# Kernel tuning notes

Hardware: AMD Instinct MI355X
Metric: run time of the kernel (lower is better)

## Reference

```python
import jax, jax.numpy as jnp
import numpy as np

HQ, HK, D = 16, 4, 64
WINDOW = 1024  # sliding-window left size; right=0 (causal)
GATE_CH = 12
RMS_EPS = 1e-8


def rms_norm(x):
    return x * jax.lax.rsqrt(jnp.mean(x * x, axis=-1, keepdims=True) + RMS_EPS)


def apply_rope(x, cos, sin):
    # x: [B,T,H,D]; cos/sin: [T,D//2] broadcast to [1,T,1,D//2]
    x1, x2 = jnp.split(x, 2, axis=-1)
    c = cos[None, :, None, :]
    s = sin[None, :, None, :]
    return jnp.concatenate([x1 * c - x2 * s, x1 * s + x2 * c], axis=-1)


def setup_inputs() -> dict:
    key = jax.random.key(0)
    ks = jax.random.split(key, 7)
    B, T, E = 2, 2048, HQ * D
    x = jax.random.normal(ks[0], (B, T, E), jnp.float32)
    value_embeds = jax.random.normal(ks[1], (B, T, HK * D), jnp.float32)
    # rope cache: angles for half the head dim
    inv_freq = 1.0 / (10000.0 ** (jnp.arange(D // 2, dtype=jnp.float32) / (D // 2)))
    ang = jnp.arange(T, dtype=jnp.float32)[:, None] * inv_freq[None, :]
    rope_cos = jnp.cos(ang)
    rope_sin = jnp.sin(ang)
    std = (3.0 ** 0.5) * (E ** -0.5)
    w_qkv = jax.random.uniform(ks[2], ((HQ + 2 * HK) * D, E), jnp.float32, -std, std)
    w_gate = jax.random.normal(ks[3], (HK, GATE_CH), jnp.float32) * 0.02
    w_o = jax.random.normal(ks[4], (E, E), jnp.float32) * 0.02
    return {"x": x, "value_embeds": value_embeds, "rope_cos": rope_cos,
            "rope_sin": rope_sin, "w_qkv": w_qkv, "w_gate": w_gate, "w_o": w_o}


def reference(x, value_embeds, rope_cos, rope_sin, w_qkv, w_gate, w_o):
    B, T, E = x.shape
    groups = HQ // HK
    qkv = jnp.einsum('bte,fe->btf', x, w_qkv).reshape(B, T, HQ + 2 * HK, D)
    q = qkv[:, :, :HQ, :]
    k = qkv[:, :, HQ:HQ + HK, :]
    v = qkv[:, :, HQ + HK:, :]
    # value-embedding gating
    ve = value_embeds.reshape(B, T, HK, D)
    gate = 3.0 * jax.nn.sigmoid(jnp.einsum('btc,hc->bth', x[..., :GATE_CH], w_gate))
    v = v + gate[..., None] * ve
    # rope + qk-norm
    q = rms_norm(apply_rope(q, rope_cos, rope_sin))
    k = rms_norm(apply_rope(k, rope_cos, rope_sin))
    # GQA: repeat kv heads
    k_rep = jnp.repeat(k, groups, axis=2)  # [B,T,HQ,D]
    v_rep = jnp.repeat(v, groups, axis=2)
    scale = 1.0 / jnp.sqrt(jnp.float32(D))
    scores = jnp.einsum('bqhd,bkhd->bhqk', q, k_rep) * scale
    i = jnp.arange(T)[:, None]
    j = jnp.arange(T)[None, :]
    mask = (j <= i) & (j >= i - WINDOW)  # causal + sliding window
    scores = jnp.where(mask[None, None], scores, jnp.float32(-1e30))
    attn = jax.nn.softmax(scores, axis=-1)
    out = jnp.einsum('bhqk,bkhd->bqhd', attn, v_rep).reshape(B, T, E)
    out = jnp.einsum('bte,fe->btf', out, w_o)
    return out
```

## Files before the change

### kernel.cpp

```cpp
#include <hip/hip_runtime.h>
#include <math.h>

#define T_LEN 2048
#define NB 2
#define E_DIM 1024
#define F_DIM 1536
#define HQn 16
#define HKn 4
#define Dh 64
#define WIN 1024
#define GATE_CH 12
#define PS 72
#define PSV 68
#define CS 73

typedef unsigned short u16;
typedef unsigned int u32;
typedef __attribute__((ext_vector_type(8))) short bf16x8;
typedef __attribute__((ext_vector_type(4))) short bf16x4;
typedef __attribute__((ext_vector_type(4))) float f32x4;

#if __has_builtin(__builtin_amdgcn_mfma_f32_16x16x16bf16_1k)
#define MFMA16(A, B, C) __builtin_amdgcn_mfma_f32_16x16x16bf16_1k(A, B, C, 0, 0, 0)
#elif __has_builtin(__builtin_amdgcn_mfma_f32_16x16x16_bf16)
#define MFMA16(A, B, C) __builtin_amdgcn_mfma_f32_16x16x16_bf16(A, B, C, 0, 0, 0)
#else
static __device__ __forceinline__ f32x4 mfma16_asm(bf16x4 a, bf16x4 b, f32x4 c) {
  f32x4 d;
  asm volatile("s_nop 1\n\tv_mfma_f32_16x16x16_bf16 %0, %1, %2, %3\n\ts_nop 7\n\ts_nop 7"
               : "=v"(d) : "v"(a), "v"(b), "v"(c));
  return d;
}
#define MFMA16(A, B, C) mfma16_asm(A, B, C)
#endif

__device__ __forceinline__ u16 f2bf(float f) {
  union { float f; unsigned int u; } v; v.f = f;
  unsigned int u = v.u + 0x7FFF + ((v.u >> 16) & 1);
  return (u16)(u >> 16);
}
__device__ __forceinline__ float bf2f(u16 h) {
  union { unsigned int u; float f; } v; v.u = ((unsigned int)h) << 16;
  return v.f;
}
__device__ __forceinline__ u32 pack_bf2(float hi, float lo) {
  union { float f; u32 u; } a, b; a.f = hi; b.f = lo;
  return __builtin_amdgcn_perm(a.u + 0x8000u, b.u + 0x8000u, 0x07060302u);
}
__device__ __forceinline__ void async_copy16(const void* g, void* l) {
  __builtin_amdgcn_global_load_lds(
      (const __attribute__((address_space(1))) unsigned int*)g,
      (__attribute__((address_space(3))) unsigned int*)l, 16, 0, 0);
}

__global__ __launch_bounds__(256) void cvt_all(
    const float4* __restrict__ x, const float4* __restrict__ wqkv,
    const float4* __restrict__ wo, uint2* __restrict__ xb,
    uint2* __restrict__ wqb, uint2* __restrict__ wob)
{
  int blk = blockIdx.x;
  const float4* in; uint2* out; int i;
  if (blk < 4096)       { in = x;    out = xb;  i = blk * 256 + threadIdx.x; }
  else if (blk < 5632)  { in = wqkv; out = wqb; i = (blk - 4096) * 256 + threadIdx.x; }
  else                  { in = wo;   out = wob; i = (blk - 5632) * 256 + threadIdx.x; }
  float4 v = in[i];
  uint2 o;
  o.x = (unsigned)f2bf(v.x) | ((unsigned)f2bf(v.y) << 16);
  o.y = (unsigned)f2bf(v.z) | ((unsigned)f2bf(v.w) << 16);
  out[i] = o;
}

__global__ __launch_bounds__(256) void gemm_qkv(
    const u16* __restrict__ A, const u16* __restrict__ B,
    const float* __restrict__ x, const float* __restrict__ ve,
    const float* __restrict__ rcos, const float* __restrict__ rsin,
    const float* __restrict__ wg,
    u16* __restrict__ qa, u16* __restrict__ ka, u16* __restrict__ vt)
{
  constexpr int K = E_DIM;
  __shared__ u16 smem[24576];
  __shared__ float gateL[128];
  u16* As = smem;
  u16* Bs = smem + 16384;
  u16* Ct = smem;
  const int tid = threadIdx.x;
  const int wave = tid >> 6, lane = tid & 63;
  const int quad = lane >> 4, lanelow = lane & 15;
  const int row0 = blockIdx.x * 128;
  const int h    = blockIdx.y;
  const int col0 = h * 64;
  const int wm = (wave >> 1) * 64, wn = (wave & 1) * 32;

  f32x4 acc[4][2];
#pragma unroll
  for (int i = 0; i < 4; ++i)
#pragma unroll
    for (int j = 0; j < 2; ++j) acc[i][j] = (f32x4){0.f, 0.f, 0.f, 0.f};

  auto stage = [&](int buf, int k0) {
#pragma unroll
    for (int s = 0; s < 4; ++s) {
      int slot = s * 256 + tid;
      int r = slot >> 3, g = (slot & 7) ^ (r & 7);
      async_copy16(A + (size_t)(row0 + r) * K + k0 + g * 8,
                   &As[buf * 8192 + slot * 8]);
    }
#pragma unroll
    for (int s = 0; s < 2; ++s) {
      int slot = s * 256 + tid;
      int r = slot >> 3, g = (slot & 7) ^ (r & 7);
      async_copy16(B + (size_t)(col0 + r) * K + k0 + g * 8,
                   &Bs[buf * 4096 + slot * 8]);
    }
  };

  stage(0, 0);
  __syncthreads();
  int cur = 0;
  for (int k0 = 0; k0 < K; k0 += 64) {
    if (k0 + 64 < K) stage(cur ^ 1, k0 + 64);
#pragma unroll
    for (int kk = 0; kk < 2; ++kk) {
      bf16x8 a[4], b[2];
#pragma unroll
      for (int i = 0; i < 4; ++i) {
        int r = wm + i * 16 + lanelow;
        a[i] = *(const bf16x8*)&As[cur * 8192 + r * 64 + (((kk * 4 + quad) ^ (r & 7)) * 8)];
      }
#pragma unroll
      for (int j = 0; j < 2; ++j) {
        int r = wn + j * 16 + lanelow;
        b[j] = *(const bf16x8*)&Bs[cur * 4096 + r * 64 + (((kk * 4 + quad) ^ (r & 7)) * 8)];
      }
#pragma unroll
      for (int i = 0; i < 4; ++i)
#pragma unroll
        for (int j = 0; j < 2; ++j)
          acc[i][j] = __builtin_amdgcn_mfma_f32_16x16x32_bf16(a[i], b[j], acc[i][j], 0, 0, 0);
    }
    __syncthreads();
    cur ^= 1;
  }

#pragma unroll
  for (int i = 0; i < 4; ++i)
#pragma unroll
    for (int j = 0; j < 2; ++j)
#pragma unroll
      for (int reg = 0; reg < 4; ++reg) {
        int row = wm + i * 16 + quad * 4 + reg;
        int col = wn + j * 16 + lanelow;
        Ct[row * CS + col] = f2bf(acc[i][j][reg]);
      }
  __syncthreads();

  if (h < HQn + HKn) {
    const bool isq = (h < HQn);
    const int half = lane & 31;
    for (int t = wave * 32; t < wave * 32 + 32; ++t) {
      int tok = row0 + t;
      int tt = tok & (T_LEN - 1);
      float c = rcos[tt * 32 + half], s = rsin[tt * 32 + half];
      float x1 = bf2f(Ct[t * CS + half]);
      float x2 = bf2f(Ct[t * CS + half + 32]);
      float y = (lane < 32) ? (x1 * c - x2 * s) : (x1 * s + x2 * c);
      float ss = y * y;
#pragma unroll
      for (int o = 32; o; o >>= 1) ss += __shfl_xor(ss, o, 64);
      float v = y * rsqrtf(ss * (1.f / Dh) + 1e-8f);
      if (isq)
        qa[((size_t)tok * HQn + h) * Dh + lane] = f2bf(v * 0.1803368801f);
      else
        ka[((size_t)tok * HKn + (h - HQn)) * Dh + lane] = f2bf(v);
    }
  } else {
    const int hk = h - (HQn + HKn);
    if (tid < 128) {
      int tok = row0 + tid;
      float g = 0.f;
#pragma unroll
      for (int c = 0; c < GATE_CH; ++c)
        g += x[(size_t)tok * E_DIM + c] * wg[hk * GATE_CH + c];
      gateL[tid] = 3.f / (1.f + __expf(-g));
    }
    __syncthreads();
    for (int t = wave * 32; t < wave * 32 + 32; ++t) {
      int tok = row0 + t;
      float val = bf2f(Ct[t * CS + lane]) +
                  gateL[t] * ve[(size_t)tok * (HKn * Dh) + hk * Dh + lane];
      Ct[t * CS + lane] = f2bf(val);
    }
    __syncthreads();
    int d = tid >> 2, tseg = (tid & 3) * 32;
    int tokbase = row0 + tseg;
    int b = tokbase >> 11;
    int tloc = tokbase & (T_LEN - 1);
    u16 tmp[32];
#pragma unroll
    for (int e = 0; e < 32; ++e) tmp[e] = Ct[(tseg + e) * CS + d];
    u16* dst = vt + ((size_t)(b * HKn + hk) * Dh + d) * T_LEN + tloc;
#pragma unroll
    for (int p = 0; p < 4; ++p)
      *(uint4*)(dst + p * 8) = *(uint4*)&tmp[p * 8];
  }
}

template<int BM, int BN, int STORE_BF16>
__global__ __launch_bounds__(256) void gemm_async(
    const u16* __restrict__ A, const u16* __restrict__ B,
    void* __restrict__ Cv, int M, int N, int K)
{
  constexpr int MI = BM / 32, NJ = BN / 32;
  constexpr int NSA = BM / 32;
  constexpr int NSB = BN / 32;
  __shared__ u16 As[2][BM * 64];
  __shared__ u16 Bs[2][BN * 64];
  const int tid = threadIdx.x;
  const int wave = tid >> 6, lane = tid & 63;
  const int quad = lane >> 4, lanelow = lane & 15;
  const int row0 = blockIdx.x * BM;
  const int col0 = blockIdx.y * BN;
  const int wm = (wave >> 1) * (BM / 2), wn = (wave & 1) * (BN / 2);

  f32x4 acc[MI][NJ];
#pragma unroll
  for (int i = 0; i < MI; ++i)
#pragma unroll
    for (int j = 0; j < NJ; ++j) acc[i][j] = (f32x4){0.f, 0.f, 0.f, 0.f};

  auto stage = [&](int buf, int k0) {
#pragma unroll
    for (int s = 0; s < NSA; ++s) {
      int slot = s * 256 + tid;
      int r = slot >> 3, g = (slot & 7) ^ (r & 7);
      async_copy16(A + (size_t)(row0 + r) * K + k0 + g * 8, &As[buf][slot * 8]);
    }
#pragma unroll
    for (int s = 0; s < NSB; ++s) {
      int slot = s * 256 + tid;
      int r = slot >> 3, g = (slot & 7) ^ (r & 7);
      async_copy16(B + (size_t)(col0 + r) * K + k0 + g * 8, &Bs[buf][slot * 8]);
    }
  };

  stage(0, 0);
  __syncthreads();
  int cur = 0;
  for (int k0 = 0; k0 < K; k0 += 64) {
    if (k0 + 64 < K) stage(cur ^ 1, k0 + 64);
#pragma unroll
    for (int kk = 0; kk < 2; ++kk) {
      bf16x8 a[MI], b[NJ];
#pragma unroll
      for (int i = 0; i < MI; ++i) {
        int r = wm + i * 16 + lanelow;
        a[i] = *(const bf16x8*)&As[cur][r * 64 + (((kk * 4 + quad) ^ (r & 7)) * 8)];
      }
#pragma unroll
      for (int j = 0; j < NJ; ++j) {
        int r = wn + j * 16 + lanelow;
        b[j] = *(const bf16x8*)&Bs[cur][r * 64 + (((kk * 4 + quad) ^ (r & 7)) * 8)];
      }
#pragma unroll
      for (int i = 0; i < MI; ++i)
#pragma unroll
        for (int j = 0; j < NJ; ++j)
          acc[i][j] = __builtin_amdgcn_mfma_f32_16x16x32_bf16(a[i], b[j], acc[i][j], 0, 0, 0);
    }
    __syncthreads();
    cur ^= 1;
  }

#pragma unroll
  for (int i = 0; i < MI; ++i)
#pragma unroll
    for (int j = 0; j < NJ; ++j) {
      int r = row0 + wm + i * 16 + quad * 4;
      int c = col0 + wn + j * 16 + lanelow;
#pragma unroll
      for (int reg = 0; reg < 4; ++reg) {
        if (STORE_BF16)
          ((u16*)Cv)[(size_t)(r + reg) * N + c] = f2bf(acc[i][j][reg]);
        else
          ((float*)Cv)[(size_t)(r + reg) * N + c] = acc[i][j][reg];
      }
    }
}

__global__ __launch_bounds__(256) void attn_mfma(
    const u16* __restrict__ qa, const u16* __restrict__ ka,
    const u16* __restrict__ vt_g, u16* __restrict__ att)
{
  __shared__ u16 Ks[2][64 * PS];
  __shared__ u16 Vt[2][64 * PSV];
  const int bx = blockIdx.x, h = blockIdx.y, b = blockIdx.z;
  const int j5 = bx & 7;
  const int t5 = (bx >> 3) & 3;
  const int tu = (t5 + (h >> 3) + 2 * b) & 3;
  const int qt = (tu == 0) ? j5
               : (tu == 1) ? (15 - j5)
                           : (16 + 2 * j5 + (tu & 1));
  const int hk = h >> 2;
  const int qb = qt * 64;
  const int tid = threadIdx.x;
  const int wave = tid >> 6, lane = tid & 63;
  const int quad = lane >> 4, lanelow = lane & 15;

  bf16x8 aQ[2];
#pragma unroll
  for (int kk = 0; kk < 2; ++kk)
    aQ[kk] = *(const bf16x8*)(qa +
        ((size_t)(b * T_LEN + qb + wave * 16 + lanelow) * HQn + h) * Dh +
        kk * 32 + quad * 8);

  f32x4 O[4];
  float l = 0.f;
#pragma unroll
  for (int dt = 0; dt < 4; ++dt) O[dt] = (f32x4){0.f, 0.f, 0.f, 0.f};

  const int kt0 = (qt >= 16) ? qt - 16 : 0;
  const int kt1 = qt;

  const int sr0 = tid >> 3,         sc0 = (tid & 7) * 8;
  const int sr1 = (tid + 256) >> 3, sc1 = ((tid + 256) & 7) * 8;
  const u16* kg = ka + (size_t)(b * T_LEN) * (HKn * Dh) + hk * Dh;
  const u16* vg = vt_g + (size_t)(b * HKn + hk) * Dh * T_LEN;

  {
    const int kb = kt0 * 64;
    uint4 k0 = *(const uint4*)(kg + (size_t)(kb + sr0) * (HKn * Dh) + sc0);
    uint4 k1 = *(const uint4*)(kg + (size_t)(kb + sr1) * (HKn * Dh) + sc1);
    uint4 v0 = *(const uint4*)(vg + (size_t)sr0 * T_LEN + kb + sc0);
    uint4 v1 = *(const uint4*)(vg + (size_t)sr1 * T_LEN + kb + sc1);
    *(uint4*)&Ks[0][sr0 * PS + sc0] = k0;
    *(uint4*)&Ks[0][sr1 * PS + sc1] = k1;
    *(uint2*)&Vt[0][sr0 * PSV + sc0]     = make_uint2(v0.x, v0.y);
    *(uint2*)&Vt[0][sr0 * PSV + sc0 + 4] = make_uint2(v0.z, v0.w);
    *(uint2*)&Vt[0][sr1 * PSV + sc1]     = make_uint2(v1.x, v1.y);
    *(uint2*)&Vt[0][sr1 * PSV + sc1 + 4] = make_uint2(v1.z, v1.w);
  }

  for (int kt = kt0; kt <= kt1; ++kt) {
    const int buf = (kt - kt0) & 1;
    const int kb = kt * 64;
    uint4 k0, k1, v0, v1;
    const bool more = (kt < kt1);
    if (more) {
      const int nb = kb + 64;
      k0 = *(const uint4*)(kg + (size_t)(nb + sr0) * (HKn * Dh) + sc0);
      k1 = *(const uint4*)(kg + (size_t)(nb + sr1) * (HKn * Dh) + sc1);
      v0 = *(const uint4*)(vg + (size_t)sr0 * T_LEN + nb + sc0);
      v1 = *(const uint4*)(vg + (size_t)sr1 * T_LEN + nb + sc1);
    }
    __syncthreads();

    f32x4 St[4];
#pragma unroll
    for (int jt = 0; jt < 4; ++jt) {
      bf16x8 aK0 = *(const bf16x8*)&Ks[buf][(jt * 16 + lanelow) * PS + quad * 8];
      bf16x8 aK1 = *(const bf16x8*)&Ks[buf][(jt * 16 + lanelow) * PS + 32 + quad * 8];
      f32x4 acc = (f32x4){-12.f, -12.f, -12.f, -12.f};
      acc = __builtin_amdgcn_mfma_f32_16x16x32_bf16(aK0, aQ[0], acc, 0, 0, 0);
      acc = __builtin_amdgcn_mfma_f32_16x16x32_bf16(aK1, aQ[1], acc, 0, 0, 0);
      St[jt] = acc;
    }
    if (kt == kt1) {
#pragma unroll
      for (int jt = 0; jt < 4; ++jt)
#pragma unroll
        for (int rr = 0; rr < 4; ++rr) {
          int ig = qb + wave * 16 + lanelow;
          int jg = kb + jt * 16 + quad * 4 + rr;
          if (jg > ig) St[jt][rr] = -1e30f;
        }
    } else if (kt == kt0 && qt >= 16) {
#pragma unroll
      for (int jt = 0; jt < 4; ++jt)
#pragma unroll
        for (int rr = 0; rr < 4; ++rr) {
          int ig = qb + wave * 16 + lanelow;
          int jg = kb + jt * 16 + quad * 4 + rr;
          if (jg < ig - WIN) St[jt][rr] = -1e30f;
        }
    }
    bf16x4 Pt[4];
#pragma unroll
    for (int jt = 0; jt < 4; ++jt) {
      float p0 = __builtin_amdgcn_exp2f(St[jt][0]);
      float p1 = __builtin_amdgcn_exp2f(St[jt][1]);
      float p2 = __builtin_amdgcn_exp2f(St[jt][2]);
      float p3 = __builtin_amdgcn_exp2f(St[jt][3]);
      l += (p0 + p1) + (p2 + p3);
      union { uint2 u; bf16x4 v; } pu;
      pu.u.x = pack_bf2(p1, p0);
      pu.u.y = pack_bf2(p3, p2);
      Pt[jt] = pu.v;
    }
#pragma unroll
    for (int dt = 0; dt < 4; ++dt)
#pragma unroll
      for (int jt = 0; jt < 4; ++jt) {
        bf16x4 aV = *(const bf16x4*)&Vt[buf][(dt * 16 + lanelow) * PSV + jt * 16 + quad * 4];
        O[dt] = MFMA16(aV, Pt[jt], O[dt]);
      }
    if (more) {
      const int nbuf = buf ^ 1;
      *(uint4*)&Ks[nbuf][sr0 * PS + sc0] = k0;
      *(uint4*)&Ks[nbuf][sr1 * PS + sc1] = k1;
      *(uint2*)&Vt[nbuf][sr0 * PSV + sc0]     = make_uint2(v0.x, v0.y);
      *(uint2*)&Vt[nbuf][sr0 * PSV + sc0 + 4] = make_uint2(v0.z, v0.w);
      *(uint2*)&Vt[nbuf][sr1 * PSV + sc1]     = make_uint2(v1.x, v1.y);
      *(uint2*)&Vt[nbuf][sr1 * PSV + sc1 + 4] = make_uint2(v1.z, v1.w);
    }
  }

  {
    float s = l;
    s += __shfl_xor(s, 16, 64);
    s += __shfl_xor(s, 32, 64);
    float inv = 1.f / s;
    int qg = qb + wave * 16 + lanelow;
    u16* obase = att + (size_t)(b * T_LEN + qg) * E_DIM + h * Dh;
#pragma unroll
    for (int dt = 0; dt < 4; ++dt) {
      bf16x4 ov;
      ov[0] = (short)f2bf(O[dt][0] * inv);
      ov[1] = (short)f2bf(O[dt][1] * inv);
      ov[2] = (short)f2bf(O[dt][2] * inv);
      ov[3] = (short)f2bf(O[dt][3] * inv);
      *(bf16x4*)(obase + dt * 16 + quad * 4) = ov;
    }
  }
}

extern "C" void kernel_launch(void* const* d_in, const int* in_sizes, int n_in,
                              void* d_out, int out_size, void* d_ws, size_t ws_size,
                              hipStream_t stream)
{
  const float* x    = (const float*)d_in[0];
  const float* ve   = (const float*)d_in[1];
  const float* rc   = (const float*)d_in[2];
  const float* rs   = (const float*)d_in[3];
  const float* wqkv = (const float*)d_in[4];
  const float* wg   = (const float*)d_in[5];
  const float* wo   = (const float*)d_in[6];
  float* out = (float*)d_out;

  char* ws = (char*)d_ws;
  u16* x_bf    = (u16*)(ws);
  u16* wqkv_bf = (u16*)(ws + 8388608);
  u16* wo_bf   = (u16*)(ws + 11534336);
  u16* q_att   = (u16*)(ws + 13631488);
  u16* k_att   = (u16*)(ws + 22020096);
  u16* v_t     = (u16*)(ws + 24117248);
  u16* att     = (u16*)(ws + 26214400);

  cvt_all<<<6656, 256, 0, stream>>>((const float4*)x, (const float4*)wqkv,
                                    (const float4*)wo, (uint2*)x_bf,
                                    (uint2*)wqkv_bf, (uint2*)wo_bf);
  gemm_qkv<<<dim3(32, 24), 256, 0, stream>>>(x_bf, wqkv_bf, x, ve, rc, rs, wg,
                                             q_att, k_att, v_t);
  attn_mfma<<<dim3(T_LEN / 64, HQn, NB), 256, 0, stream>>>(q_att, k_att, v_t, att);
  gemm_async<128, 64, 0><<<dim3(32, 16), 256, 0, stream>>>(
      att, wo_bf, out, 4096, E_DIM, E_DIM);
}
```

Measured before the change: 163.0 us.

## Use 4-stage async-copy pipeline with single barrier per k-step in both GEMMs

Both the QKV and output-projection GEMMs move from a double-buffered 64-wide K loop with two __syncthreads per step to a 4-buffer ring of 32-wide K tiles. Three tiles are kept in flight, with explicit vmcnt waits and one s_barrier per iteration. The XOR swizzle is dropped in favour of a plain 32-element row layout, and setprio is raised around the MFMA block. The aim is to hide global-load latency and cut barrier overhead, at the cost of possible LDS bank conflicts from the unswizzled layout.

New measurement: 168.6 us. 1.03x slower.

```diff
diff --git a/kernel.cpp b/kernel.cpp
--- a/kernel.cpp
+++ b/kernel.cpp
@@ -78,6 +78,7 @@
     u16* __restrict__ qa, u16* __restrict__ ka, u16* __restrict__ vt)
 {
   constexpr int K = E_DIM;
+  constexpr int NT = K / 32;
   __shared__ u16 smem[24576];
   __shared__ float gateL[128];
   u16* As = smem;
@@ -97,51 +98,51 @@
 #pragma unroll
     for (int j = 0; j < 2; ++j) acc[i][j] = (f32x4){0.f, 0.f, 0.f, 0.f};
 
-  auto stage = [&](int buf, int k0) {
-#pragma unroll
-    for (int s = 0; s < 4; ++s) {
-      int slot = s * 256 + tid;
-      int r = slot >> 3, g = (slot & 7) ^ (r & 7);
-      async_copy16(A + (size_t)(row0 + r) * K + k0 + g * 8,
-                   &As[buf * 8192 + slot * 8]);
-    }
-#pragma unroll
-    for (int s = 0; s < 2; ++s) {
-      int slot = s * 256 + tid;
-      int r = slot >> 3, g = (slot & 7) ^ (r & 7);
-      async_copy16(B + (size_t)(col0 + r) * K + k0 + g * 8,
-                   &Bs[buf * 4096 + slot * 8]);
-    }
+  const int rr = tid >> 2, gg = (tid & 3) * 8;
+  const u16* aSrc0 = A + (size_t)(row0 + rr) * K + gg;
+  const u16* aSrc1 = A + (size_t)(row0 + 64 + rr) * K + gg;
+  const u16* bSrc  = B + (size_t)(col0 + rr) * K + gg;
+  u16* aDst0 = As + tid * 8;
+  u16* aDst1 = As + (256 + tid) * 8;
+  u16* bDst  = Bs + tid * 8;
+
+  auto stage = [&](int t) {
+    const int buf = t & 3;
+    const int ke = t * 32;
+    async_copy16(aSrc0 + ke, aDst0 + buf * 4096);
+    async_copy16(aSrc1 + ke, aDst1 + buf * 4096);
+    async_copy16(bSrc  + ke, bDst  + buf * 2048);
   };
 
-  stage(0, 0);
+  const int aO0 = (wm + lanelow) * 32 + quad * 8;
+  const int bO0 = (wn + lanelow) * 32 + quad * 8;
+
+  stage(0); stage(1); stage(2);
+  for (int t = 0; t < NT; ++t) {
+    if (t < NT - 2)       asm volatile("s_waitcnt vmcnt(6)" ::: "memory");
+    else if (t == NT - 2) asm volatile("s_waitcnt vmcnt(3)" ::: "memory");
+    else                  asm volatile("s_waitcnt vmcnt(0)" ::: "memory");
+    __builtin_amdgcn_s_barrier();
+    __builtin_amdgcn_sched_barrier(0);
+    if (t + 3 < NT) stage(t + 3);
+    const int bufA = (t & 3) * 4096, bufB = (t & 3) * 2048;
+    bf16x8 a[4], b[2];
+#pragma unroll
+    for (int i = 0; i < 4; ++i)
+      a[i] = *(const bf16x8*)&As[bufA + aO0 + i * 512];
+#pragma unroll
+    for (int j = 0; j < 2; ++j)
+      b[j] = *(const bf16x8*)&Bs[bufB + bO0 + j * 512];
+    __builtin_amdgcn_s_setprio(1);
+#pragma unroll
+    for (int i = 0; i < 4; ++i)
+#pragma unroll
+      for (int j = 0; j < 2; ++j)
+        acc[i][j] = __builtin_amdgcn_mfma_f32_16x16x32_bf16(a[i], b[j], acc[i][j], 0, 0, 0);
+    __builtin_amdgcn_s_setprio(0);
+  }
+
   __syncthreads();
-  int cur = 0;
-  for (int k0 = 0; k0 < K; k0 += 64) {
-    if (k0 + 64 < K) stage(cur ^ 1, k0 + 64);
-#pragma unroll
-    for (int kk = 0; kk < 2; ++kk) {
-      bf16x8 a[4], b[2];
-#pragma unroll
-      for (int i = 0; i < 4; ++i) {
-        int r = wm + i * 16 + lanelow;
-        a[i] = *(const bf16x8*)&As[cur * 8192 + r * 64 + (((kk * 4 + quad) ^ (r & 7)) * 8)];
-      }
-#pragma unroll
-      for (int j = 0; j < 2; ++j) {
-        int r = wn + j * 16 + lanelow;
-        b[j] = *(const bf16x8*)&Bs[cur * 4096 + r * 64 + (((kk * 4 + quad) ^ (r & 7)) * 8)];
-      }
-#pragma unroll
-      for (int i = 0; i < 4; ++i)
-#pragma unroll
-        for (int j = 0; j < 2; ++j)
-          acc[i][j] = __builtin_amdgcn_mfma_f32_16x16x32_bf16(a[i], b[j], acc[i][j], 0, 0, 0);
-    }
-    __syncthreads();
-    cur ^= 1;
-  }
-
 #pragma unroll
   for (int i = 0; i < 4; ++i)
 #pragma unroll
@@ -205,85 +206,80 @@
   }
 }
 
-template<int BM, int BN, int STORE_BF16>
-__global__ __launch_bounds__(256) void gemm_async(
+__global__ __launch_bounds__(256) void gemm_wo(
     const u16* __restrict__ A, const u16* __restrict__ B,
-    void* __restrict__ Cv, int M, int N, int K)
+    float* __restrict__ C, int N, int K)
 {
-  constexpr int MI = BM / 32, NJ = BN / 32;
-  constexpr int NSA = BM / 32;
-  constexpr int NSB = BN / 32;
-  __shared__ u16 As[2][BM * 64];
-  __shared__ u16 Bs[2][BN * 64];
+  const int NT = K / 32;
+  __shared__ u16 smem[24576];
+  u16* As = smem;
+  u16* Bs = smem + 16384;
   const int tid = threadIdx.x;
   const int wave = tid >> 6, lane = tid & 63;
   const int quad = lane >> 4, lanelow = lane & 15;
-  const int row0 = blockIdx.x * BM;
-  const int col0 = blockIdx.y * BN;
-  const int wm = (wave >> 1) * (BM / 2), wn = (wave & 1) * (BN / 2);
-
-  f32x4 acc[MI][NJ];
-#pragma unroll
-  for (int i = 0; i < MI; ++i)
-#pragma unroll
-    for (int j = 0; j < NJ; ++j) acc[i][j] = (f32x4){0.f, 0.f, 0.f, 0.f};
-
-  auto stage = [&](int buf, int k0) {
-#pragma unroll
-    for (int s = 0; s < NSA; ++s) {
-      int slot = s * 256 + tid;
-      int r = slot >> 3, g = (slot & 7) ^ (r & 7);
-      async_copy16(A + (size_t)(row0 + r) * K + k0 + g * 8, &As[buf][slot * 8]);
-    }
-#pragma unroll
-    for (int s = 0; s < NSB; ++s) {
-      int slot = s * 256 + tid;
-      int r = slot >> 3, g = (slot & 7) ^ (r & 7);
-      async_copy16(B + (size_t)(col0 + r) * K + k0 + g * 8, &Bs[buf][slot * 8]);
-    }
+  const int row0 = blockIdx.x * 128;
+  const int col0 = blockIdx.y * 64;
+  const int wm = (wave >> 1) * 64, wn = (wave & 1) * 32;
+
+  f32x4 acc[4][2];
+#pragma unroll
+  for (int i = 0; i < 4; ++i)
+#pragma unroll
+    for (int j = 0; j < 2; ++j) acc[i][j] = (f32x4){0.f, 0.f, 0.f, 0.f};
+
+  const int rr = tid >> 2, gg = (tid & 3) * 8;
+  const u16* aSrc0 = A + (size_t)(row0 + rr) * K + gg;
+  const u16* aSrc1 = A + (size_t)(row0 + 64 + rr) * K + gg;
+  const u16* bSrc  = B + (size_t)(col0 + rr) * K + gg;
+  u16* aDst0 = As + tid * 8;
+  u16* aDst1 = As + (256 + tid) * 8;
+  u16* bDst  = Bs + tid * 8;
+
+  auto stage = [&](int t) {
+    const int buf = t & 3;
+    const int ke = t * 32;
+    async_copy16(aSrc0 + ke, aDst0 + buf * 4096);
+    async_copy16(aSrc1 + ke, aDst1 + buf * 4096);
+    async_copy16(bSrc  + ke, bDst  + buf * 2048);
   };
 
-  stage(0, 0);
-  __syncthreads();
-  int cur = 0;
-  for (int k0 = 0; k0 < K; k0 += 64) {
-    if (k0 + 64 < K) stage(cur ^ 1, k0 + 64);
-#pragma unroll
-    for (int kk = 0; kk < 2; ++kk) {
-      bf16x8 a[MI], b[NJ];
-#pragma unroll
-      for (int i = 0; i < MI; ++i) {
-        int r = wm + i * 16 + lanelow;
-        a[i] = *(const bf16x8*)&As[cur][r * 64 + (((kk * 4 + quad) ^ (r & 7)) * 8)];
-      }
-#pragma unroll
-      for (int j = 0; j < NJ; ++j) {
-        int r = wn + j * 16 + lanelow;
-        b[j] = *(const bf16x8*)&Bs[cur][r * 64 + (((kk * 4 + quad) ^ (r & 7)) * 8)];
-      }
-#pragma unroll
-      for (int i = 0; i < MI; ++i)
-#pragma unroll
-        for (int j = 0; j < NJ; ++j)
-          acc[i][j] = __builtin_amdgcn_mfma_f32_16x16x32_bf16(a[i], b[j], acc[i][j], 0, 0, 0);
-    }
-    __syncthreads();
-    cur ^= 1;
-  }
-
-#pragma unroll
-  for (int i = 0; i < MI; ++i)
-#pragma unroll
-    for (int j = 0; j < NJ; ++j) {
+  const int aO0 = (wm + lanelow) * 32 + quad * 8;
+  const int bO0 = (wn + lanelow) * 32 + quad * 8;
+
+  stage(0); stage(1); stage(2);
+  for (int t = 0; t < NT; ++t) {
+    if (t < NT - 2)       asm volatile("s_waitcnt vmcnt(6)" ::: "memory");
+    else if (t == NT - 2) asm volatile("s_waitcnt vmcnt(3)" ::: "memory");
+    else                  asm volatile("s_waitcnt vmcnt(0)" ::: "memory");
+    __builtin_amdgcn_s_barrier();
+    __builtin_amdgcn_sched_barrier(0);
+    if (t + 3 < NT) stage(t + 3);
+    const int bufA = (t & 3) * 4096, bufB = (t & 3) * 2048;
+    bf16x8 a[4], b[2];
+#pragma unroll
+    for (int i = 0; i < 4; ++i)
+      a[i] = *(const bf16x8*)&As[bufA + aO0 + i * 512];
+#pragma unroll
+    for (int j = 0; j < 2; ++j)
+      b[j] = *(const bf16x8*)&Bs[bufB + bO0 + j * 512];
+    __builtin_amdgcn_s_setprio(1);
+#pragma unroll
+    for (int i = 0; i < 4; ++i)
+#pragma unroll
+      for (int j = 0; j < 2; ++j)
+        acc[i][j] = __builtin_amdgcn_mfma_f32_16x16x32_bf16(a[i], b[j], acc[i][j], 0, 0, 0);
+    __builtin_amdgcn_s_setprio(0);
+  }
+
+#pragma unroll
+  for (int i = 0; i < 4; ++i)
+#pragma unroll
+    for (int j = 0; j < 2; ++j) {
       int r = row0 + wm + i * 16 + quad * 4;
       int c = col0 + wn + j * 16 + lanelow;
 #pragma unroll
-      for (int reg = 0; reg < 4; ++reg) {
-        if (STORE_BF16)
-          ((u16*)Cv)[(size_t)(r + reg) * N + c] = f2bf(acc[i][j][reg]);
-        else
-          ((float*)Cv)[(size_t)(r + reg) * N + c] = acc[i][j][reg];
-      }
+      for (int reg = 0; reg < 4; ++reg)
+        C[(size_t)(r + reg) * N + c] = acc[i][j][reg];
     }
 }
 
@@ -461,6 +457,5 @@
   gemm_qkv<<<dim3(32, 24), 256, 0, stream>>>(x_bf, wqkv_bf, x, ve, rc, rs, wg,
                                              q_att, k_att, v_t);
   attn_mfma<<<dim3(T_LEN / 64, HQn, NB), 256, 0, stream>>>(q_att, k_att, v_t, att);
-  gemm_async<128, 64, 0><<<dim3(32, 16), 256, 0, stream>>>(
-      att, wo_bf, out, 4096, E_DIM, E_DIM);
-}
+  gemm_wo<<<dim3(32, 16), 256, 0, stream>>>(att, wo_bf, out, E_DIM, E_DIM);
+}
```
